# Performance work log

Hardware: AMD Instinct MI355X
Metric: run time of the kernel (lower is better)

The kernel has to match this reference:

```python
import jax, jax.numpy as jnp
import numpy as np

POSE_IDS = np.array([0, 4, 8, 12, 16])
BN_EPS = 1e-5


def setup_inputs() -> dict:
    key = jax.random.key(0)
    ks = jax.random.split(key, 8)
    N, C, H, W = 64, 2048, 24, 12
    P, Cl = 5, 256
    Cm = C + P * Cl  # 3328
    return {
        "x": jax.random.normal(ks[0], (N, C, H, W), jnp.float32),
        "poses": jax.random.uniform(ks[1], (N, 17, 4), jnp.float32),
        "local_w": jax.random.normal(ks[2], (P, Cl, C), jnp.float32) * 0.02,
        "local_b": jnp.zeros((P, Cl), jnp.float32),
        "local_gamma": jnp.ones((P, Cl), jnp.float32),
        "local_beta": jnp.zeros((P, Cl), jnp.float32),
        "local_mean": jax.random.normal(ks[3], (P, Cl), jnp.float32) * 0.1,
        "local_var": jax.random.uniform(ks[4], (P, Cl), jnp.float32, 0.5, 1.5),
        "merge_w": jax.random.normal(ks[5], (C, Cm), jnp.float32) * 0.02,
        "merge_b": jnp.zeros((C,), jnp.float32),
        "merge_gamma": jnp.ones((C,), jnp.float32),
        "merge_beta": jnp.zeros((C,), jnp.float32),
        "merge_mean": jax.random.normal(ks[6], (C,), jnp.float32) * 0.1,
        "merge_var": jax.random.uniform(ks[7], (C,), jnp.float32, 0.5, 1.5),
    }


def reference(x, poses, local_w, local_b, local_gamma, local_beta, local_mean,
              local_var, merge_w, merge_b, merge_gamma, merge_beta, merge_mean,
              merge_var):
    N, C, H, W = x.shape
    kp = poses[:, jnp.asarray(POSE_IDS), :]  # [N,P,4]
    # box = [left, top, w, h]; clamp to [0, 0.75]; scale whole box by confidence
    half = jnp.full_like(kp[..., 0], 0.5)
    box = jnp.stack([kp[..., 0] - 0.25, kp[..., 1] - 0.25, half, half], axis=-1)
    box = jnp.clip(box, 0.0, 0.75) * kp[..., 2:3]
    # integer ROI bounds on the feature grid (round-half-to-even like torch)
    xs = jnp.maximum(0, jnp.round(W * box[..., 0])).astype(jnp.int32)          # [N,P]
    xe = jnp.minimum(W - 1, jnp.round(W * (box[..., 0] + box[..., 2]))).astype(jnp.int32)
    ys = jnp.maximum(0, jnp.round(H * box[..., 1])).astype(jnp.int32)
    ye = jnp.minimum(H - 1, jnp.round(H * (box[..., 1] + box[..., 3]))).astype(jnp.int32)
    rows = jnp.arange(H)
    cols = jnp.arange(W)
    mh = (rows[None, None, :] >= ys[..., None]) & (rows[None, None, :] < ye[..., None])  # [N,P,H]
    mw = (cols[None, None, :] >= xs[..., None]) & (cols[None, None, :] < xe[..., None])  # [N,P,W]
    mask = (mh[..., :, None] & mw[..., None, :]).astype(x.dtype)  # [N,P,H,W]
    # masked average pool over the ROI (single pass over x)
    sums = jnp.einsum('nchw,nphw->npc', x, mask)
    area = ((ye - ys) * (xe - xs)).astype(x.dtype)
    avg = sums / jnp.where(area > 0, area, 1.0)[..., None]  # [N,P,C], 0 for empty ROIs
    # per-part 1x1 conv + BN(eval) + ReLU -> [N,P,Cl]
    loc = jnp.einsum('npc,pkc->npk', avg, local_w) + local_b[None]
    loc = (loc - local_mean[None]) * (local_gamma[None] / jnp.sqrt(local_var[None] + BN_EPS)) + local_beta[None]
    loc = jax.nn.relu(loc)
    # global max pool -> [N,C]
    gfeat = x.max(axis=(2, 3))
    cat = jnp.concatenate([loc.reshape(N, -1), gfeat], axis=1)  # [N, P*Cl + C]
    # merge 1x1 conv + BN(eval) + ReLU
    y = cat @ merge_w.T + merge_b
    y = (y - merge_mean) * (merge_gamma / jnp.sqrt(merge_var + BN_EPS)) + merge_beta
    y = jax.nn.relu(y)
    # F.normalize(p=2, dim=1)
    norm = jnp.linalg.norm(y, axis=1, keepdims=True)
    return y / jnp.maximum(norm, 1e-12)
```

## Files before the change

kernel.cpp:

```cpp
#include <hip/hip_runtime.h>

#define N_   64
#define C_   2048
#define HW_  288
#define P_   5
#define CM_  3328
#define LOC_ 1280
#define SEGC 8
#define SEGM 13

#define PITCH 28

__global__ __launch_bounds__(256) void kB(const float* __restrict__ x,
    const float* __restrict__ poses,
    float* __restrict__ avg, float* __restrict__ cat) {
  __shared__ float lds[2][256 * PITCH];
  const int t  = threadIdx.x;
  const int n  = blockIdx.x >> 3;
  const int cb = (blockIdx.x & 7) << 8;
  const int chbase = n * C_ + cb;

  unsigned MH[P_], MW[P_];
  float INV[P_];
  const float* kpn = poses + (size_t)n * 68;
#pragma unroll
  for (int p = 0; p < P_; ++p) {
    const float* kp = kpn + 16 * p;
    float px = kp[0], py = kp[1], z = kp[2];
    float bx = fminf(fmaxf(px - 0.25f, 0.f), 0.75f) * z;
    float by = fminf(fmaxf(py - 0.25f, 0.f), 0.75f) * z;
    float bw = 0.5f * z;
    float bh = 0.5f * z;
    int xs = (int)fmaxf(0.f,  rintf(12.f * bx));
    int xe = (int)fminf(11.f, rintf(12.f * (bx + bw)));
    int ys = (int)fmaxf(0.f,  rintf(24.f * by));
    int ye = (int)fminf(23.f, rintf(24.f * (by + bh)));
    MH[p] = ((1u << ye) - 1u) & ~((1u << ys) - 1u);
    MW[p] = ((1u << xe) - 1u) & ~((1u << xs) - 1u);
    int area = (ye - ys) * (xe - xs);
    INV[p] = area > 0 ? 1.f / (float)area : 1.f;
  }

  const float4* x4 = (const float4*)x;
  auto stage = [&](int ci, int db) {
#pragma unroll
    for (int k = 0; k < 6; ++k) {
      unsigned flat = k * 256 + t;
      unsigned cl = flat / 6u;
      unsigned j  = flat - 6u * cl;
      float4 v = x4[(size_t)(chbase + cl) * 72 + ci * 6 + j];
      *(float4*)&lds[db][cl * PITCH + 4 * j] = v;
    }
  };

  float s[P_] = {0.f, 0.f, 0.f, 0.f, 0.f};
  float mx = -3.402823466e+38f;

  stage(0, 0);
  __syncthreads();
  for (int ci = 0; ci < 12; ++ci) {
    if (ci + 1 < 12) stage(ci + 1, (ci + 1) & 1);
    const float* row = &lds[ci & 1][t * PITCH];
#pragma unroll
    for (int r = 0; r < 2; ++r) {
      int h = 2 * ci + r;
      float4 a = *(const float4*)(row + r * 12 + 0);
      float4 b = *(const float4*)(row + r * 12 + 4);
      float4 c = *(const float4*)(row + r * 12 + 8);
      float m1 = fmaxf(fmaxf(a.x, a.y), fmaxf(a.z, a.w));
      float m2 = fmaxf(fmaxf(b.x, b.y), fmaxf(b.z, b.w));
      float m3 = fmaxf(fmaxf(c.x, c.y), fmaxf(c.z, c.w));
      mx = fmaxf(mx, fmaxf(m1, fmaxf(m2, m3)));
#pragma unroll
      for (int p = 0; p < P_; ++p) {
        unsigned cm = ((MH[p] >> h) & 1u) ? MW[p] : 0u;
        if (cm) {
          float t0 = ((cm & 0x001u) ? a.x : 0.f) + ((cm & 0x002u) ? a.y : 0.f);
          float t1 = ((cm & 0x004u) ? a.z : 0.f) + ((cm & 0x008u) ? a.w : 0.f);
          float t2 = ((cm & 0x010u) ? b.x : 0.f) + ((cm & 0x020u) ? b.y : 0.f);
          float t3 = ((cm & 0x040u) ? b.z : 0.f) + ((cm & 0x080u) ? b.w : 0.f);
          float t4 = ((cm & 0x100u) ? c.x : 0.f) + ((cm & 0x200u) ? c.y : 0.f);
          float t5 = ((cm & 0x400u) ? c.z : 0.f) + ((cm & 0x800u) ? c.w : 0.f);
          s[p] += ((t0 + t1) + (t2 + t3)) + (t4 + t5);
        }
      }
    }
    __syncthreads();
  }

  int c = cb + t;
  cat[(size_t)n * CM_ + LOC_ + c] = mx;
#pragma unroll
  for (int p = 0; p < P_; ++p)
    avg[((size_t)n * P_ + p) * C_ + c] = s[p] * INV[p];
}

template<int GSEG>
__device__ __forceinline__ void gemm_tile(const float* __restrict__ Ag, int lda,
                                          const float* __restrict__ Wg, int ldw,
                                          float* __restrict__ Og, int ldo,
                                          float* As, float* Ws) {
  const int t  = threadIdx.x;
  const int nq = t & 15;
  const int kq = t >> 4;
  const int c4 = (t & 15) << 2;
  const int rr = t >> 4;
  float4 pA[4], pW[4];
#pragma unroll
  for (int i = 0; i < 4; ++i) {
    int r = rr + (i << 4);
    pA[i] = *(const float4*)&Ag[(size_t)r * lda + c4];
    pW[i] = *(const float4*)&Wg[(size_t)r * ldw + c4];
  }
  float acc[4][4] = {};
  for (int g = 0; g < GSEG; ++g) {
    __syncthreads();
#pragma unroll
    for (int i = 0; i < 4; ++i) {
      int r = rr + (i << 4);
      *(float4*)&As[r * 68 + c4] = pA[i];
      *(float4*)&Ws[r * 68 + c4] = pW[i];
    }
    __syncthreads();
    if (g + 1 < GSEG) {
#pragma unroll
      for (int i = 0; i < 4; ++i) {
        int r = rr + (i << 4);
        pA[i] = *(const float4*)&Ag[(size_t)r * lda + ((g + 1) << 6) + c4];
        pW[i] = *(const float4*)&Wg[(size_t)r * ldw + ((g + 1) << 6) + c4];
      }
    }
#pragma unroll
    for (int c = 0; c < 64; c += 4) {
      float4 a[4], w[4];
#pragma unroll
      for (int i = 0; i < 4; ++i) a[i] = *(const float4*)&As[(nq + (i << 4)) * 68 + c];
#pragma unroll
      for (int j = 0; j < 4; ++j) w[j] = *(const float4*)&Ws[(kq + (j << 4)) * 68 + c];
#pragma unroll
      for (int i = 0; i < 4; ++i)
#pragma unroll
        for (int j = 0; j < 4; ++j)
          acc[i][j] += a[i].x * w[j].x + a[i].y * w[j].y + a[i].z * w[j].z + a[i].w * w[j].w;
    }
  }
#pragma unroll
  for (int i = 0; i < 4; ++i)
#pragma unroll
    for (int j = 0; j < 4; ++j)
      Og[(size_t)(nq + (i << 4)) * ldo + kq + (j << 4)] = acc[i][j];
}

__global__ __launch_bounds__(256) void kC(const float* __restrict__ avg,
                                          const float* __restrict__ local_w,
                                          float* __restrict__ locP) {
  __shared__ float As[64 * 68];
  __shared__ float Ws[64 * 68];
  int b  = blockIdx.x;
  int tl = b >> 3;
  int sg = b & 7;
  int p  = tl >> 2;
  int kt = tl & 3;
  const float* Ag = avg + p * C_ + (sg << 8);
  const float* Wg = local_w + ((size_t)p * 256 + (kt << 6)) * C_ + (sg << 8);
  float* Og = locP + (size_t)sg * (N_ * LOC_) + (p << 8) + (kt << 6);
  gemm_tile<4>(Ag, P_ * C_, Wg, C_, Og, LOC_, As, Ws);
}

__global__ __launch_bounds__(256) void kC2(const float* __restrict__ locP,
    const float* __restrict__ lb, const float* __restrict__ lg, const float* __restrict__ lbe,
    const float* __restrict__ lm, const float* __restrict__ lv,
    float* __restrict__ cat) {
  int i = blockIdx.x * 256 + threadIdx.x;
  int n = i / LOC_;
  int q = i - n * LOC_;
  float s = 0.f;
#pragma unroll
  for (int sg = 0; sg < SEGC; ++sg) s += locP[(size_t)sg * (N_ * LOC_) + i];
  float sc = lg[q] / sqrtf(lv[q] + 1e-5f);
  float v = (s + lb[q] - lm[q]) * sc + lbe[q];
  cat[(size_t)n * CM_ + q] = fmaxf(v, 0.f);
}

__global__ __launch_bounds__(256) void kD(const float* __restrict__ cat,
                                          const float* __restrict__ merge_w,
                                          float* __restrict__ mrgP) {
  __shared__ float As[64 * 68];
  __shared__ float Ws[64 * 68];
  int b  = blockIdx.x;
  int jt = b / SEGM;
  int sg = b - jt * SEGM;
  const float* Ag = cat + (sg << 8);
  const float* Wg = merge_w + (size_t)(jt << 6) * CM_ + (sg << 8);
  float* Og = mrgP + (size_t)sg * (N_ * C_) + (jt << 6);
  gemm_tile<4>(Ag, CM_, Wg, CM_, Og, C_, As, Ws);
}

__global__ __launch_bounds__(256) void kE(const float* __restrict__ mrgP,
    const float* __restrict__ mb, const float* __restrict__ mg, const float* __restrict__ mbe,
    const float* __restrict__ mm, const float* __restrict__ mv,
    float* __restrict__ out) {
  int n = blockIdx.x, t = threadIdx.x;
  float z[8]; float ss = 0.f;
#pragma unroll
  for (int r = 0; r < 8; ++r) {
    int j = t + (r << 8);
    float y = 0.f;
#pragma unroll
    for (int sg = 0; sg < SEGM; ++sg) y += mrgP[(size_t)sg * (N_ * C_) + (size_t)n * C_ + j];
    float sc = mg[j] / sqrtf(mv[j] + 1e-5f);
    float v = (y + mb[j] - mm[j]) * sc + mbe[j];
    v = fmaxf(v, 0.f);
    z[r] = v; ss += v * v;
  }
#pragma unroll
  for (int off = 32; off; off >>= 1) ss += __shfl_xor(ss, off, 64);
  __shared__ float red[4];
  if ((t & 63) == 0) red[t >> 6] = ss;
  __syncthreads();
  float tot = red[0] + red[1] + red[2] + red[3];
  float inv = 1.f / fmaxf(sqrtf(tot), 1e-12f);
#pragma unroll
  for (int r = 0; r < 8; ++r) out[(size_t)n * C_ + t + (r << 8)] = z[r] * inv;
}

extern "C" void kernel_launch(void* const* d_in, const int* in_sizes, int n_in,
                              void* d_out, int out_size, void* d_ws, size_t ws_size,
                              hipStream_t stream) {
  const float* x          = (const float*)d_in[0];
  const float* poses      = (const float*)d_in[1];
  const float* local_w    = (const float*)d_in[2];
  const float* local_b    = (const float*)d_in[3];
  const float* local_g    = (const float*)d_in[4];
  const float* local_be   = (const float*)d_in[5];
  const float* local_m    = (const float*)d_in[6];
  const float* local_v    = (const float*)d_in[7];
  const float* merge_w    = (const float*)d_in[8];
  const float* merge_b    = (const float*)d_in[9];
  const float* merge_g    = (const float*)d_in[10];
  const float* merge_be   = (const float*)d_in[11];
  const float* merge_m    = (const float*)d_in[12];
  const float* merge_v    = (const float*)d_in[13];

  float* ws   = (float*)d_ws;
  float* cat  = ws;
  float* avg  = ws + 212992;
  float* locP = ws + 868352;
  float* mrgP = ws + 1523712;

  kB<<<512, 256, 0, stream>>>(x, poses, avg, cat);
  kC<<<20 * SEGC, 256, 0, stream>>>(avg, local_w, locP);
  kC2<<<(N_ * LOC_) / 256, 256, 0, stream>>>(locP, local_b, local_g, local_be,
                                             local_m, local_v, cat);
  kD<<<32 * SEGM, 256, 0, stream>>>(cat, merge_w, mrgP);
  kE<<<N_, 256, 0, stream>>>(mrgP, merge_b, merge_g, merge_be, merge_m, merge_v,
                             (float*)d_out);
}
```

Baseline: 341.7 us.

## Prefetch pooling tiles into registers and drop register prefetch in GEMM tile

In the pooling kernel, the next chunk of x is now loaded into registers before computing on the current LDS buffer and written to LDS afterwards, with precomputed global and LDS offsets. This lets global-load latency overlap with compute and takes the index math out of the loop. In the GEMM tile helper the opposite happens: the register prefetch of the next K-slice is removed and tiles are copied straight from global to LDS each iteration. That lowers register pressure but exposes load latency.

```diff
diff --git a/kernel.cpp b/kernel.cpp
--- a/kernel.cpp
+++ b/kernel.cpp
@@ -42,24 +42,35 @@
   }
 
   const float4* x4 = (const float4*)x;
-  auto stage = [&](int ci, int db) {
-#pragma unroll
-    for (int k = 0; k < 6; ++k) {
-      unsigned flat = k * 256 + t;
-      unsigned cl = flat / 6u;
-      unsigned j  = flat - 6u * cl;
-      float4 v = x4[(size_t)(chbase + cl) * 72 + ci * 6 + j];
-      *(float4*)&lds[db][cl * PITCH + 4 * j] = v;
-    }
+  size_t gbase[6];
+  int    loff[6];
+#pragma unroll
+  for (int k = 0; k < 6; ++k) {
+    unsigned flat = k * 256 + t;
+    unsigned cl = flat / 6u;
+    unsigned j  = flat - 6u * cl;
+    gbase[k] = (size_t)(chbase + cl) * 72 + j;
+    loff[k]  = cl * PITCH + 4 * j;
+  }
+
+  float4 rg[6];
+  auto loadRegs = [&](int ci) {
+#pragma unroll
+    for (int k = 0; k < 6; ++k) rg[k] = x4[gbase[k] + ci * 6];
+  };
+  auto writeRegs = [&](int db) {
+#pragma unroll
+    for (int k = 0; k < 6; ++k) *(float4*)&lds[db][loff[k]] = rg[k];
   };
 
   float s[P_] = {0.f, 0.f, 0.f, 0.f, 0.f};
   float mx = -3.402823466e+38f;
 
-  stage(0, 0);
+  loadRegs(0);
+  writeRegs(0);
   __syncthreads();
   for (int ci = 0; ci < 12; ++ci) {
-    if (ci + 1 < 12) stage(ci + 1, (ci + 1) & 1);
+    if (ci + 1 < 12) loadRegs(ci + 1);
     const float* row = &lds[ci & 1][t * PITCH];
 #pragma unroll
     for (int r = 0; r < 2; ++r) {
@@ -85,7 +96,10 @@
         }
       }
     }
-    __syncthreads();
+    if (ci + 1 < 12) {
+      writeRegs((ci + 1) & 1);
+      __syncthreads();
+    }
   }
 
   int c = cb + t;
@@ -105,31 +119,16 @@
   const int kq = t >> 4;
   const int c4 = (t & 15) << 2;
   const int rr = t >> 4;
-  float4 pA[4], pW[4];
-#pragma unroll
-  for (int i = 0; i < 4; ++i) {
-    int r = rr + (i << 4);
-    pA[i] = *(const float4*)&Ag[(size_t)r * lda + c4];
-    pW[i] = *(const float4*)&Wg[(size_t)r * ldw + c4];
-  }
   float acc[4][4] = {};
   for (int g = 0; g < GSEG; ++g) {
     __syncthreads();
 #pragma unroll
     for (int i = 0; i < 4; ++i) {
       int r = rr + (i << 4);
-      *(float4*)&As[r * 68 + c4] = pA[i];
-      *(float4*)&Ws[r * 68 + c4] = pW[i];
+      *(float4*)&As[r * 68 + c4] = *(const float4*)&Ag[(size_t)r * lda + (g << 6) + c4];
+      *(float4*)&Ws[r * 68 + c4] = *(const float4*)&Wg[(size_t)r * ldw + (g << 6) + c4];
     }
     __syncthreads();
-    if (g + 1 < GSEG) {
-#pragma unroll
-      for (int i = 0; i < 4; ++i) {
-        int r = rr + (i << 4);
-        pA[i] = *(const float4*)&Ag[(size_t)r * lda + ((g + 1) << 6) + c4];
-        pW[i] = *(const float4*)&Wg[(size_t)r * ldw + ((g + 1) << 6) + c4];
-      }
-    }
 #pragma unroll
     for (int c = 0; c < 64; c += 4) {
       float4 a[4], w[4];
```

Result: no change. 335.2 us (-1.9%).
